# Kernel optimization log

Hardware: AMD Instinct MI355X
Metric: run time of the kernel (lower is better)

Reference implementation:

```python
import jax, jax.numpy as jnp
import numpy as np


def setup_inputs() -> dict:
    key = jax.random.key(0)
    ks = jax.random.split(key, 5)
    S, B, H, L = 512, 64, 1024, 2
    scale = 0.1
    return {
        "x": jax.random.normal(ks[0], (S, B, H), dtype=jnp.float32),
        "h0": jnp.zeros((L, B, H), dtype=jnp.float32),
        "c0": jnp.zeros((L, B, H), dtype=jnp.float32),
        "Wx": jax.random.uniform(ks[1], (L, 4 * H, H), minval=-scale, maxval=scale, dtype=jnp.float32),
        "Wh": jax.random.uniform(ks[2], (L, 4 * H, H), minval=-scale, maxval=scale, dtype=jnp.float32),
        "bx": jax.random.uniform(ks[3], (L, 4 * H), minval=-scale, maxval=scale, dtype=jnp.float32),
        "bh": jax.random.uniform(ks[4], (L, 4 * H), minval=-scale, maxval=scale, dtype=jnp.float32),
    }


def _cell(x_t, h_prev, c_prev, Wx_l, Wh_l, bx_l, bh_l, H):
    # gates: [B, 4H]; chunk order per source: f, i, o, c_ex
    gates = x_t @ Wx_l.T + bx_l + h_prev @ Wh_l.T + bh_l
    f, i, o, c_ex = jnp.split(gates, 4, axis=1)
    f = jax.nn.sigmoid(f)
    i = jax.nn.sigmoid(i)
    o = jax.nn.sigmoid(o)
    c_ex = jnp.tanh(c_ex)
    c = f * c_prev + i * c_ex
    h = o * jnp.tanh(c)
    return h, c


def reference(x, h0, c0, Wx, Wh, bx, bh):
    # x: [S, B, H]; h0/c0: [L, B, H]; Wx/Wh: [L, 4H, H]; bx/bh: [L, 4H]
    L = h0.shape[0]
    H = h0.shape[-1]

    def step(carry, x_t):
        h_all, c_all = carry  # each [L, B, H]
        out = x_t
        hs, cs = [], []
        for l in range(L):  # small fixed layer count
            h, c = _cell(out, h_all[l], c_all[l], Wx[l], Wh[l], bx[l], bh[l], H)
            out = h  # dropout is identity in eval mode
            hs.append(h)
            cs.append(c)
        return (jnp.stack(hs, 0), jnp.stack(cs, 0)), out

    (h_fin, c_fin), ys = jax.lax.scan(step, (h0, c0), x)
    return ys, (h_fin, c_fin)
```

## Files before the change

kernel.cpp:

```cpp
#include <hip/hip_runtime.h>

typedef __bf16 bf16_t;
typedef __bf16 bf16x8 __attribute__((ext_vector_type(8)));
typedef __bf16 bf16x4 __attribute__((ext_vector_type(4)));
typedef float  f32x4  __attribute__((ext_vector_type(4)));
typedef unsigned long long u64;

#define S_LEN 512
#define BATCH 64
#define HID 1024
#define BH (BATCH*HID)
#define G4 (4*HID)
#define NBLK 256
#define LBLK 128
#define NTHR 512
#define CSTRIDE 16

__device__ __forceinline__ float sigmoid_f(float x) { return 1.f / (1.f + __expf(-x)); }
__device__ __forceinline__ float tanh_f(float x) {
    float e = __expf(-2.f * fabsf(x));
    float t = (1.f - e) / (1.f + e);
    return x >= 0.f ? t : -t;
}

__device__ __forceinline__ bf16x8 cvt8(const float* p) {
    float4 a = *reinterpret_cast<const float4*>(p);
    float4 b = *reinterpret_cast<const float4*>(p + 4);
    bf16x8 r;
    r[0] = (bf16_t)a.x; r[1] = (bf16_t)a.y; r[2] = (bf16_t)a.z; r[3] = (bf16_t)a.w;
    r[4] = (bf16_t)b.x; r[5] = (bf16_t)b.y; r[6] = (bf16_t)b.z; r[7] = (bf16_t)b.w;
    return r;
}

__device__ __forceinline__ void wait_layer(const unsigned* w, unsigned thr, int lane) {
    const unsigned* p0 = w + (size_t)lane * CSTRIDE;
    const unsigned* p1 = w + (size_t)(64 + lane) * CSTRIDE;
    for (;;) {
        unsigned a = __hip_atomic_load(p0, __ATOMIC_RELAXED, __HIP_MEMORY_SCOPE_AGENT);
        unsigned b = __hip_atomic_load(p1, __ATOMIC_RELAXED, __HIP_MEMORY_SCOPE_AGENT);
        if (__all((int)(a >= thr && b >= thr))) break;
        __builtin_amdgcn_s_sleep(1);
    }
    asm volatile("" ::: "memory");
}

__device__ __forceinline__ void wait_dual(const unsigned* w0, unsigned thr0,
                                          const unsigned* w1, unsigned thr1, int lane) {
    const unsigned* p00 = w0 + (size_t)lane * CSTRIDE;
    const unsigned* p01 = w0 + (size_t)(64 + lane) * CSTRIDE;
    const unsigned* p10 = w1 + (size_t)lane * CSTRIDE;
    const unsigned* p11 = w1 + (size_t)(64 + lane) * CSTRIDE;
    for (;;) {
        unsigned a = __hip_atomic_load(p00, __ATOMIC_RELAXED, __HIP_MEMORY_SCOPE_AGENT);
        unsigned b = __hip_atomic_load(p01, __ATOMIC_RELAXED, __HIP_MEMORY_SCOPE_AGENT);
        unsigned c = __hip_atomic_load(p10, __ATOMIC_RELAXED, __HIP_MEMORY_SCOPE_AGENT);
        unsigned d = __hip_atomic_load(p11, __ATOMIC_RELAXED, __HIP_MEMORY_SCOPE_AGENT);
        if (__all((int)(a >= thr0 && b >= thr0 && c >= thr1 && d >= thr1))) break;
        __builtin_amdgcn_s_sleep(1);
    }
    asm volatile("" ::: "memory");
}

__global__ void prep_kernel(const float* __restrict__ h0,
                            bf16_t* __restrict__ h0buf, bf16_t* __restrict__ h1buf,
                            unsigned* __restrict__ dw, int mask0, int mask1) {
    int gtid = blockIdx.x * blockDim.x + threadIdx.x;
    int gsz  = gridDim.x * blockDim.x;
    if (gtid < 2 * LBLK) dw[gtid * CSTRIDE] = 0u;
    for (int i = gtid; i < BH; i += gsz) {
        h0buf[(size_t)mask0 * BH + i] = (bf16_t)h0[i];
        h1buf[(size_t)mask1 * BH + i] = (bf16_t)h0[BH + i];
    }
}

__global__ __launch_bounds__(NTHR, 2) void lstm_persistent(
    const float* __restrict__ x,
    const float* __restrict__ c0,
    const float* __restrict__ Wx,
    const float* __restrict__ Wh,
    const float* __restrict__ bx,
    const float* __restrict__ bh,
    float* __restrict__ out,
    bf16_t* __restrict__ h0buf,
    bf16_t* __restrict__ h1buf,
    unsigned* __restrict__ dw,
    int ff, int mask0, int mask1)
{
    __shared__ __attribute__((aligned(16))) unsigned char lds_w[256 * 512];
    __shared__ __attribute__((aligned(16))) float lds_red[8 * 256];
    __shared__ __attribute__((aligned(16))) float lds_hf[BATCH * 8];

    const int tid  = threadIdx.x;
    const int bid  = blockIdx.x;
    const int l    = bid >> 7;
    const int ug8  = bid & 127;
    const int lane = tid & 63;
    const int wv   = tid >> 6;
    const int mt   = wv >> 1;
    const int kh   = wv & 1;
    const int quad = lane >> 4;
    const int r16  = lane & 15;

    float* ys   = out;
    float* hfin = out + (size_t)S_LEN * BH;
    float* cfin = hfin + 2 * BH;

    {
        const float* WxL = Wx + (size_t)l * G4 * HID;
        const float* WhL = Wh + (size_t)l * G4 * HID;
        for (int ch = tid; ch < 32 * 256; ch += NTHR) {
            int row = ch & 31;
            int gr  = ch >> 5;
            int ul = row >> 2, g = row & 3;
            size_t R = (size_t)g * HID + 8 * ug8 + ul;
            const float* src = (gr < 128) ? (WxL + R * HID + (size_t)gr * 8)
                                          : (WhL + R * HID + (size_t)(gr - 128) * 8);
            *reinterpret_cast<bf16x8*>(&lds_w[gr * 512 + row * 16]) = cvt8(src);
        }
    }

    const int b_loc  = lane >> 2;
    const int uu     = lane & 3;
    const int b_glob = 16 * mt + b_loc;
    const int u_loc  = 4 * kh + uu;
    const int u_glob = 8 * ug8 + u_loc;

    float bias_r[4];
    #pragma unroll
    for (int gi = 0; gi < 4; ++gi) {
        int R = gi * HID + u_glob;
        bias_r[gi] = bx[l * G4 + R] + bh[l * G4 + R];
    }
    float c_reg = c0[(size_t)l * BH + (size_t)b_glob * HID + u_glob];

    bf16_t* pubbuf = (l == 0) ? h0buf : h1buf;
    const int pubmask = (l == 0) ? mask0 : mask1;
    const unsigned* dw0 = dw;
    const unsigned* dw1 = dw + LBLK * CSTRIDE;
    unsigned* myword = &dw[(l * LBLK + ug8) * CSTRIDE];
    __syncthreads();

    const int arow_off = (16 * mt + r16) * HID + kh * 512 + quad * 8;

    bf16x8 axp[16];
    if (l == 0) {
        const float* arow = x + arow_off;
        #pragma unroll
        for (int ks = 0; ks < 16; ++ks) axp[ks] = cvt8(arow + ks * 32);
    }

    for (int t = 0; t < S_LEN; ++t) {
        f32x4 acc0 = {0.f, 0.f, 0.f, 0.f};
        f32x4 acc1 = {0.f, 0.f, 0.f, 0.f};

        if (l == 0) {
            #pragma unroll
            for (int ks = 0; ks < 16; ++ks) {
                int gr = kh * 64 + ks * 4 + quad;
                bf16x8 b0 = *reinterpret_cast<const bf16x8*>(&lds_w[gr * 512 + r16 * 16]);
                bf16x8 b1 = *reinterpret_cast<const bf16x8*>(&lds_w[gr * 512 + (16 + r16) * 16]);
                acc0 = __builtin_amdgcn_mfma_f32_16x16x32_bf16(axp[ks], b0, acc0, 0, 0, 0);
                acc1 = __builtin_amdgcn_mfma_f32_16x16x32_bf16(axp[ks], b1, acc1, 0, 0, 0);
            }
            if (t + 1 < S_LEN) {
                const float* arow = x + (size_t)(t + 1) * BH + arow_off;
                #pragma unroll
                for (int ks = 0; ks < 16; ++ks) axp[ks] = cvt8(arow + ks * 32);
            }
            wait_layer(dw0, (unsigned)t, lane);
            if (!ff) __builtin_amdgcn_fence(__ATOMIC_ACQUIRE, "agent");
            const bf16_t* ah = h0buf + (size_t)((t - 1) & mask0) * BH + arow_off;
            bf16x8 af[16];
            #pragma unroll
            for (int ks = 0; ks < 16; ++ks)
                af[ks] = *reinterpret_cast<const bf16x8*>(ah + ks * 32);
            #pragma unroll
            for (int ks = 0; ks < 16; ++ks) {
                int gr = 128 + kh * 64 + ks * 4 + quad;
                bf16x8 b0 = *reinterpret_cast<const bf16x8*>(&lds_w[gr * 512 + r16 * 16]);
                bf16x8 b1 = *reinterpret_cast<const bf16x8*>(&lds_w[gr * 512 + (16 + r16) * 16]);
                acc0 = __builtin_amdgcn_mfma_f32_16x16x32_bf16(af[ks], b0, acc0, 0, 0, 0);
                acc1 = __builtin_amdgcn_mfma_f32_16x16x32_bf16(af[ks], b1, acc1, 0, 0, 0);
            }
        } else {
            wait_dual(dw0, (unsigned)(t + 1), dw1, (unsigned)t, lane);
            if (!ff) __builtin_amdgcn_fence(__ATOMIC_ACQUIRE, "agent");
            const bf16_t* ah = h1buf + (size_t)((t - 1) & mask1) * BH + arow_off;
            const bf16_t* ax = h0buf + (size_t)(t & mask0) * BH + arow_off;
            bf16x8 ahf[16], axf[16];
            #pragma unroll
            for (int ks = 0; ks < 16; ++ks)
                ahf[ks] = *reinterpret_cast<const bf16x8*>(ah + ks * 32);
            #pragma unroll
            for (int ks = 0; ks < 16; ++ks)
                axf[ks] = *reinterpret_cast<const bf16x8*>(ax + ks * 32);
            #pragma unroll
            for (int ks = 0; ks < 16; ++ks) {
                int gr = 128 + kh * 64 + ks * 4 + quad;
                bf16x8 b0 = *reinterpret_cast<const bf16x8*>(&lds_w[gr * 512 + r16 * 16]);
                bf16x8 b1 = *reinterpret_cast<const bf16x8*>(&lds_w[gr * 512 + (16 + r16) * 16]);
                acc0 = __builtin_amdgcn_mfma_f32_16x16x32_bf16(ahf[ks], b0, acc0, 0, 0, 0);
                acc1 = __builtin_amdgcn_mfma_f32_16x16x32_bf16(ahf[ks], b1, acc1, 0, 0, 0);
            }
            #pragma unroll
            for (int ks = 0; ks < 16; ++ks) {
                int gr = kh * 64 + ks * 4 + quad;
                bf16x8 b0 = *reinterpret_cast<const bf16x8*>(&lds_w[gr * 512 + r16 * 16]);
                bf16x8 b1 = *reinterpret_cast<const bf16x8*>(&lds_w[gr * 512 + (16 + r16) * 16]);
                acc0 = __builtin_amdgcn_mfma_f32_16x16x32_bf16(axf[ks], b0, acc0, 0, 0, 0);
                acc1 = __builtin_amdgcn_mfma_f32_16x16x32_bf16(axf[ks], b1, acc1, 0, 0, 0);
            }
        }

        {
            f32x4 ship = kh ? acc0 : acc1;
            *reinterpret_cast<f32x4*>(&lds_red[wv * 256 + lane * 4]) = ship;
            __syncthreads();
            f32x4 part = *reinterpret_cast<const f32x4*>(&lds_red[(wv ^ 1) * 256 + lane * 4]);
            f32x4 keep = kh ? acc1 : acc0;
            acc0 = keep + part;
        }

        {
            const int quad_s = b_loc >> 2;
            const int reg_s  = b_loc & 3;
            float gsum[4];
            #pragma unroll
            for (int gi = 0; gi < 4; ++gi) {
                int lane_s = (quad_s << 4) | (4 * uu + gi);
                float v0 = __shfl(acc0[0], lane_s, 64);
                float v1 = __shfl(acc0[1], lane_s, 64);
                float v2 = __shfl(acc0[2], lane_s, 64);
                float v3 = __shfl(acc0[3], lane_s, 64);
                float v  = (reg_s == 0) ? v0 : (reg_s == 1) ? v1 : (reg_s == 2) ? v2 : v3;
                gsum[gi] = v + bias_r[gi];
            }
            float fg = sigmoid_f(gsum[0]);
            float ig = sigmoid_f(gsum[1]);
            float og = sigmoid_f(gsum[2]);
            float cx = tanh_f(gsum[3]);
            float cN = fg * c_reg + ig * cx;
            float h  = og * tanh_f(cN);
            c_reg = cN;
            lds_hf[b_glob * 8 + u_loc] = h;
            if (t == S_LEN - 1) {
                hfin[(size_t)l * BH + (size_t)b_glob * HID + u_glob] = h;
                cfin[(size_t)l * BH + (size_t)b_glob * HID + u_glob] = cN;
            }
        }
        __syncthreads();

        if (tid < 64) {
            if (!ff && l == 0 && t >= 8) {
                const unsigned thr = (unsigned)(t - 6);
                for (;;) {
                    unsigned v0 = __hip_atomic_load(&dw1[lane * CSTRIDE],
                                                    __ATOMIC_RELAXED, __HIP_MEMORY_SCOPE_AGENT);
                    unsigned v1 = __hip_atomic_load(&dw1[(64 + lane) * CSTRIDE],
                                                    __ATOMIC_RELAXED, __HIP_MEMORY_SCOPE_AGENT);
                    if (__all((int)(v0 >= thr && v1 >= thr))) break;
                    __builtin_amdgcn_s_sleep(1);
                }
            }
            const float* hp = &lds_hf[lane * 8];
            union { bf16x4 v; u64 q; } p0, p1;
            #pragma unroll
            for (int j = 0; j < 4; ++j) {
                p0.v[j] = (bf16_t)hp[j];
                p1.v[j] = (bf16_t)hp[4 + j];
            }
            bf16_t* dst = pubbuf + (size_t)(t & pubmask) * BH + (size_t)lane * HID + 8 * ug8;
            __hip_atomic_store((u64*)(void*)dst,       p0.q, __ATOMIC_RELAXED, __HIP_MEMORY_SCOPE_AGENT);
            __hip_atomic_store((u64*)(void*)(dst + 4), p1.q, __ATOMIC_RELAXED, __HIP_MEMORY_SCOPE_AGENT);
            asm volatile("s_waitcnt vmcnt(0)" ::: "memory");
            if (lane == 0)
                __hip_atomic_store(myword, (unsigned)(t + 1),
                                   __ATOMIC_RELAXED, __HIP_MEMORY_SCOPE_AGENT);
            if (l == 1) {
                float* yd = ys + (size_t)t * BH + (size_t)lane * HID + 8 * ug8;
                __builtin_nontemporal_store(*reinterpret_cast<const f32x4*>(hp),     reinterpret_cast<f32x4*>(yd));
                __builtin_nontemporal_store(*reinterpret_cast<const f32x4*>(hp + 4), reinterpret_cast<f32x4*>(yd + 4));
            }
        }
    }
}

extern "C" void kernel_launch(void* const* d_in, const int* in_sizes, int n_in,
                              void* d_out, int out_size, void* d_ws, size_t ws_size,
                              hipStream_t stream) {
    (void)in_sizes; (void)n_in; (void)out_size;
    const float* x  = (const float*)d_in[0];
    const float* h0 = (const float*)d_in[1];
    const float* c0 = (const float*)d_in[2];
    const float* Wx = (const float*)d_in[3];
    const float* Wh = (const float*)d_in[4];
    const float* bx = (const float*)d_in[5];
    const float* bh = (const float*)d_in[6];

    unsigned char* ws = (unsigned char*)d_ws;
    unsigned* dw = (unsigned*)ws;
    size_t off = 32768;
    size_t need_ff = off + (size_t)2 * S_LEN * BH * 2;
    int ff, mask0, mask1;
    bf16_t *h0buf, *h1buf;
    if (ws_size >= need_ff) {
        ff = 1; mask0 = S_LEN - 1; mask1 = S_LEN - 1;
        h0buf = (bf16_t*)(ws + off); off += (size_t)S_LEN * BH * 2;
        h1buf = (bf16_t*)(ws + off);
    } else {
        ff = 0; mask0 = 7; mask1 = 1;
        h0buf = (bf16_t*)(ws + off); off += (size_t)8 * BH * 2;
        h1buf = (bf16_t*)(ws + off);
    }

    prep_kernel<<<2048, 256, 0, stream>>>(h0, h0buf, h1buf, dw, mask0, mask1);
    lstm_persistent<<<NBLK, NTHR, 0, stream>>>(x, c0, Wx, Wh, bx, bh, (float*)d_out,
                                               h0buf, h1buf, dw, ff, mask0, mask1);
}
```

Measured before the change: 6.746 ms.

## Centralize inter-block flag polling in one wave and pack flags densely

Counter flags are packed contiguously instead of padded to 64-byte strides, so a poll touches fewer cache lines. A single wave now polls all global readiness flags and releases the rest of the block through an LDS generation word, where before every wave polled global memory. The layer-0 backpressure wait on layer 1 moves from the publish phase into this same pre-step poll. This cuts global atomic polling traffic, but the other waves now spin on LDS and rely on LDS ordering, and writers of neighbouring flags now share cache lines.

```diff
diff --git a/kernel.cpp b/kernel.cpp
--- a/kernel.cpp
+++ b/kernel.cpp
@@ -14,7 +14,6 @@
 #define NBLK 256
 #define LBLK 128
 #define NTHR 512
-#define CSTRIDE 16
 
 __device__ __forceinline__ float sigmoid_f(float x) { return 1.f / (1.f + __expf(-x)); }
 __device__ __forceinline__ float tanh_f(float x) {
@@ -32,41 +31,12 @@
     return r;
 }
 
-__device__ __forceinline__ void wait_layer(const unsigned* w, unsigned thr, int lane) {
-    const unsigned* p0 = w + (size_t)lane * CSTRIDE;
-    const unsigned* p1 = w + (size_t)(64 + lane) * CSTRIDE;
-    for (;;) {
-        unsigned a = __hip_atomic_load(p0, __ATOMIC_RELAXED, __HIP_MEMORY_SCOPE_AGENT);
-        unsigned b = __hip_atomic_load(p1, __ATOMIC_RELAXED, __HIP_MEMORY_SCOPE_AGENT);
-        if (__all((int)(a >= thr && b >= thr))) break;
-        __builtin_amdgcn_s_sleep(1);
-    }
-    asm volatile("" ::: "memory");
-}
-
-__device__ __forceinline__ void wait_dual(const unsigned* w0, unsigned thr0,
-                                          const unsigned* w1, unsigned thr1, int lane) {
-    const unsigned* p00 = w0 + (size_t)lane * CSTRIDE;
-    const unsigned* p01 = w0 + (size_t)(64 + lane) * CSTRIDE;
-    const unsigned* p10 = w1 + (size_t)lane * CSTRIDE;
-    const unsigned* p11 = w1 + (size_t)(64 + lane) * CSTRIDE;
-    for (;;) {
-        unsigned a = __hip_atomic_load(p00, __ATOMIC_RELAXED, __HIP_MEMORY_SCOPE_AGENT);
-        unsigned b = __hip_atomic_load(p01, __ATOMIC_RELAXED, __HIP_MEMORY_SCOPE_AGENT);
-        unsigned c = __hip_atomic_load(p10, __ATOMIC_RELAXED, __HIP_MEMORY_SCOPE_AGENT);
-        unsigned d = __hip_atomic_load(p11, __ATOMIC_RELAXED, __HIP_MEMORY_SCOPE_AGENT);
-        if (__all((int)(a >= thr0 && b >= thr0 && c >= thr1 && d >= thr1))) break;
-        __builtin_amdgcn_s_sleep(1);
-    }
-    asm volatile("" ::: "memory");
-}
-
 __global__ void prep_kernel(const float* __restrict__ h0,
                             bf16_t* __restrict__ h0buf, bf16_t* __restrict__ h1buf,
                             unsigned* __restrict__ dw, int mask0, int mask1) {
     int gtid = blockIdx.x * blockDim.x + threadIdx.x;
     int gsz  = gridDim.x * blockDim.x;
-    if (gtid < 2 * LBLK) dw[gtid * CSTRIDE] = 0u;
+    if (gtid < 2 * LBLK) dw[gtid] = 0u;
     for (int i = gtid; i < BH; i += gsz) {
         h0buf[(size_t)mask0 * BH + i] = (bf16_t)h0[i];
         h1buf[(size_t)mask1 * BH + i] = (bf16_t)h0[BH + i];
@@ -89,6 +59,7 @@
     __shared__ __attribute__((aligned(16))) unsigned char lds_w[256 * 512];
     __shared__ __attribute__((aligned(16))) float lds_red[8 * 256];
     __shared__ __attribute__((aligned(16))) float lds_hf[BATCH * 8];
+    __shared__ unsigned lds_go;
 
     const int tid  = threadIdx.x;
     const int bid  = blockIdx.x;
@@ -104,6 +75,8 @@
     float* ys   = out;
     float* hfin = out + (size_t)S_LEN * BH;
     float* cfin = hfin + 2 * BH;
+
+    if (tid == 0) lds_go = 0u;
 
     {
         const float* WxL = Wx + (size_t)l * G4 * HID;
@@ -136,8 +109,8 @@
     bf16_t* pubbuf = (l == 0) ? h0buf : h1buf;
     const int pubmask = (l == 0) ? mask0 : mask1;
     const unsigned* dw0 = dw;
-    const unsigned* dw1 = dw + LBLK * CSTRIDE;
-    unsigned* myword = &dw[(l * LBLK + ug8) * CSTRIDE];
+    const unsigned* dw1 = dw + LBLK;
+    unsigned* myword = &dw[l * LBLK + ug8];
     __syncthreads();
 
     const int arow_off = (16 * mt + r16) * HID + kh * 512 + quad * 8;
@@ -152,6 +125,7 @@
     for (int t = 0; t < S_LEN; ++t) {
         f32x4 acc0 = {0.f, 0.f, 0.f, 0.f};
         f32x4 acc1 = {0.f, 0.f, 0.f, 0.f};
+        const unsigned gen = (unsigned)t + 1u;
 
         if (l == 0) {
             #pragma unroll
@@ -167,8 +141,39 @@
                 #pragma unroll
                 for (int ks = 0; ks < 16; ++ks) axp[ks] = cvt8(arow + ks * 32);
             }
-            wait_layer(dw0, (unsigned)t, lane);
-            if (!ff) __builtin_amdgcn_fence(__ATOMIC_ACQUIRE, "agent");
+        }
+
+        if (wv == 7) {
+            unsigned thr0, thr1;
+            if (l == 0) {
+                thr0 = (unsigned)t;
+                thr1 = (!ff && t >= 8) ? (unsigned)(t - 6) : 0u;
+            } else {
+                thr0 = (unsigned)(t + 1);
+                thr1 = (unsigned)t;
+            }
+            const unsigned* q0 = dw0 + lane;
+            const unsigned* q1 = dw0 + 64 + lane;
+            const unsigned* q2 = dw1 + lane;
+            const unsigned* q3 = dw1 + 64 + lane;
+            for (;;) {
+                unsigned a = __hip_atomic_load(q0, __ATOMIC_RELAXED, __HIP_MEMORY_SCOPE_AGENT);
+                unsigned b = __hip_atomic_load(q1, __ATOMIC_RELAXED, __HIP_MEMORY_SCOPE_AGENT);
+                unsigned c = __hip_atomic_load(q2, __ATOMIC_RELAXED, __HIP_MEMORY_SCOPE_AGENT);
+                unsigned d = __hip_atomic_load(q3, __ATOMIC_RELAXED, __HIP_MEMORY_SCOPE_AGENT);
+                if (__all((int)(a >= thr0 && b >= thr0 && c >= thr1 && d >= thr1))) break;
+                __builtin_amdgcn_s_sleep(1);
+            }
+            __hip_atomic_store(&lds_go, gen, __ATOMIC_RELAXED, __HIP_MEMORY_SCOPE_WORKGROUP);
+        } else {
+            while (__hip_atomic_load(&lds_go, __ATOMIC_RELAXED,
+                                     __HIP_MEMORY_SCOPE_WORKGROUP) < gen)
+                __builtin_amdgcn_s_sleep(1);
+        }
+        asm volatile("" ::: "memory");
+        if (!ff) __builtin_amdgcn_fence(__ATOMIC_ACQUIRE, "agent");
+
+        if (l == 0) {
             const bf16_t* ah = h0buf + (size_t)((t - 1) & mask0) * BH + arow_off;
             bf16x8 af[16];
             #pragma unroll
@@ -183,8 +188,6 @@
                 acc1 = __builtin_amdgcn_mfma_f32_16x16x32_bf16(af[ks], b1, acc1, 0, 0, 0);
             }
         } else {
-            wait_dual(dw0, (unsigned)(t + 1), dw1, (unsigned)t, lane);
-            if (!ff) __builtin_amdgcn_fence(__ATOMIC_ACQUIRE, "agent");
             const bf16_t* ah = h1buf + (size_t)((t - 1) & mask1) * BH + arow_off;
             const bf16_t* ax = h0buf + (size_t)(t & mask0) * BH + arow_off;
             bf16x8 ahf[16], axf[16];
@@ -251,17 +254,6 @@
         __syncthreads();
 
         if (tid < 64) {
-            if (!ff && l == 0 && t >= 8) {
-                const unsigned thr = (unsigned)(t - 6);
-                for (;;) {
-                    unsigned v0 = __hip_atomic_load(&dw1[lane * CSTRIDE],
-                                                    __ATOMIC_RELAXED, __HIP_MEMORY_SCOPE_AGENT);
-                    unsigned v1 = __hip_atomic_load(&dw1[(64 + lane) * CSTRIDE],
-                                                    __ATOMIC_RELAXED, __HIP_MEMORY_SCOPE_AGENT);
-                    if (__all((int)(v0 >= thr && v1 >= thr))) break;
-                    __builtin_amdgcn_s_sleep(1);
-                }
-            }
             const float* hp = &lds_hf[lane * 8];
             union { bf16x4 v; u64 q; } p0, p1;
             #pragma unroll
@@ -274,8 +266,7 @@
             __hip_atomic_store((u64*)(void*)(dst + 4), p1.q, __ATOMIC_RELAXED, __HIP_MEMORY_SCOPE_AGENT);
             asm volatile("s_waitcnt vmcnt(0)" ::: "memory");
             if (lane == 0)
-                __hip_atomic_store(myword, (unsigned)(t + 1),
-                                   __ATOMIC_RELAXED, __HIP_MEMORY_SCOPE_AGENT);
+                __hip_atomic_store(myword, gen, __ATOMIC_RELAXED, __HIP_MEMORY_SCOPE_AGENT);
             if (l == 1) {
                 float* yd = ys + (size_t)t * BH + (size_t)lane * HID + 8 * ug8;
                 __builtin_nontemporal_store(*reinterpret_cast<const f32x4*>(hp),     reinterpret_cast<f32x4*>(yd));
```

Result: slower. 7.551 ms (+11.9%).

## Move layer-1 back-pressure wait and ys stores off the publish critical path

Applied to the files above, without the earlier changes.

Folds layer 0's ring-buffer back-pressure wait on layer 1 into the existing pre-GEMM dual wait, so the single publishing wave no longer spins after the barrier. Each layer-1 thread keeps its h value and writes ys for the previous step after the loads of the next step are issued, so the output stores overlap with the next step's MFMA work instead of delaying the publish path. It also shrinks the flag stride and reorders the x prefetch after the h loads, with sched barriers to pin the order. Risks include extra shuffles, flags sharing cache lines now that the stride is smaller, and ordering subtleties in the added wait.

```diff
diff --git a/kernel.cpp b/kernel.cpp
--- a/kernel.cpp
+++ b/kernel.cpp
@@ -14,7 +14,7 @@
 #define NBLK 256
 #define LBLK 128
 #define NTHR 512
-#define CSTRIDE 16
+#define CSTRIDE 4
 
 __device__ __forceinline__ float sigmoid_f(float x) { return 1.f / (1.f + __expf(-x)); }
 __device__ __forceinline__ float tanh_f(float x) {
@@ -148,10 +148,12 @@
         #pragma unroll
         for (int ks = 0; ks < 16; ++ks) axp[ks] = cvt8(arow + ks * 32);
     }
+    float h_prev = 0.f;
 
     for (int t = 0; t < S_LEN; ++t) {
         f32x4 acc0 = {0.f, 0.f, 0.f, 0.f};
         f32x4 acc1 = {0.f, 0.f, 0.f, 0.f};
+        const unsigned gen = (unsigned)t + 1u;
 
         if (l == 0) {
             #pragma unroll
@@ -162,18 +164,21 @@
                 acc0 = __builtin_amdgcn_mfma_f32_16x16x32_bf16(axp[ks], b0, acc0, 0, 0, 0);
                 acc1 = __builtin_amdgcn_mfma_f32_16x16x32_bf16(axp[ks], b1, acc1, 0, 0, 0);
             }
+            unsigned thrg = (!ff && t >= 8) ? (unsigned)(t - 6) : 0u;
+            if (thrg) wait_dual(dw0, (unsigned)t, dw1, thrg, lane);
+            else      wait_layer(dw0, (unsigned)t, lane);
+            if (!ff) __builtin_amdgcn_fence(__ATOMIC_ACQUIRE, "agent");
+            const bf16_t* ah = h0buf + (size_t)((t - 1) & mask0) * BH + arow_off;
+            bf16x8 af[16];
+            #pragma unroll
+            for (int ks = 0; ks < 16; ++ks)
+                af[ks] = *reinterpret_cast<const bf16x8*>(ah + ks * 32);
             if (t + 1 < S_LEN) {
                 const float* arow = x + (size_t)(t + 1) * BH + arow_off;
                 #pragma unroll
                 for (int ks = 0; ks < 16; ++ks) axp[ks] = cvt8(arow + ks * 32);
             }
-            wait_layer(dw0, (unsigned)t, lane);
-            if (!ff) __builtin_amdgcn_fence(__ATOMIC_ACQUIRE, "agent");
-            const bf16_t* ah = h0buf + (size_t)((t - 1) & mask0) * BH + arow_off;
-            bf16x8 af[16];
-            #pragma unroll
-            for (int ks = 0; ks < 16; ++ks)
-                af[ks] = *reinterpret_cast<const bf16x8*>(ah + ks * 32);
+            __builtin_amdgcn_sched_barrier(0);
             #pragma unroll
             for (int ks = 0; ks < 16; ++ks) {
                 int gr = 128 + kh * 64 + ks * 4 + quad;
@@ -194,6 +199,19 @@
             #pragma unroll
             for (int ks = 0; ks < 16; ++ks)
                 axf[ks] = *reinterpret_cast<const bf16x8*>(ax + ks * 32);
+            if (t > 0) {
+                f32x4 yv;
+                yv[0] = h_prev;
+                yv[1] = __shfl_xor(h_prev, 1, 64);
+                yv[2] = __shfl_xor(h_prev, 2, 64);
+                yv[3] = __shfl_xor(h_prev, 3, 64);
+                if (uu == 0) {
+                    float* yd = ys + (size_t)(t - 1) * BH + (size_t)b_glob * HID
+                              + 8 * ug8 + 4 * kh;
+                    __builtin_nontemporal_store(yv, reinterpret_cast<f32x4*>(yd));
+                }
+            }
+            __builtin_amdgcn_sched_barrier(0);
             #pragma unroll
             for (int ks = 0; ks < 16; ++ks) {
                 int gr = 128 + kh * 64 + ks * 4 + quad;
@@ -242,6 +260,7 @@
             float cN = fg * c_reg + ig * cx;
             float h  = og * tanh_f(cN);
             c_reg = cN;
+            h_prev = h;
             lds_hf[b_glob * 8 + u_loc] = h;
             if (t == S_LEN - 1) {
                 hfin[(size_t)l * BH + (size_t)b_glob * HID + u_glob] = h;
@@ -251,17 +270,6 @@
         __syncthreads();
 
         if (tid < 64) {
-            if (!ff && l == 0 && t >= 8) {
-                const unsigned thr = (unsigned)(t - 6);
-                for (;;) {
-                    unsigned v0 = __hip_atomic_load(&dw1[lane * CSTRIDE],
-                                                    __ATOMIC_RELAXED, __HIP_MEMORY_SCOPE_AGENT);
-                    unsigned v1 = __hip_atomic_load(&dw1[(64 + lane) * CSTRIDE],
-                                                    __ATOMIC_RELAXED, __HIP_MEMORY_SCOPE_AGENT);
-                    if (__all((int)(v0 >= thr && v1 >= thr))) break;
-                    __builtin_amdgcn_s_sleep(1);
-                }
-            }
             const float* hp = &lds_hf[lane * 8];
             union { bf16x4 v; u64 q; } p0, p1;
             #pragma unroll
@@ -274,13 +282,20 @@
             __hip_atomic_store((u64*)(void*)(dst + 4), p1.q, __ATOMIC_RELAXED, __HIP_MEMORY_SCOPE_AGENT);
             asm volatile("s_waitcnt vmcnt(0)" ::: "memory");
             if (lane == 0)
-                __hip_atomic_store(myword, (unsigned)(t + 1),
-                                   __ATOMIC_RELAXED, __HIP_MEMORY_SCOPE_AGENT);
-            if (l == 1) {
-                float* yd = ys + (size_t)t * BH + (size_t)lane * HID + 8 * ug8;
-                __builtin_nontemporal_store(*reinterpret_cast<const f32x4*>(hp),     reinterpret_cast<f32x4*>(yd));
-                __builtin_nontemporal_store(*reinterpret_cast<const f32x4*>(hp + 4), reinterpret_cast<f32x4*>(yd + 4));
-            }
+                __hip_atomic_store(myword, gen, __ATOMIC_RELAXED, __HIP_MEMORY_SCOPE_AGENT);
+        }
+    }
+
+    if (l == 1) {
+        f32x4 yv;
+        yv[0] = h_prev;
+        yv[1] = __shfl_xor(h_prev, 1, 64);
+        yv[2] = __shfl_xor(h_prev, 2, 64);
+        yv[3] = __shfl_xor(h_prev, 3, 64);
+        if (uu == 0) {
+            float* yd = ys + (size_t)(S_LEN - 1) * BH + (size_t)b_glob * HID
+                      + 8 * ug8 + 4 * kh;
+            __builtin_nontemporal_store(yv, reinterpret_cast<f32x4*>(yd));
         }
     }
 }
```

Result: slower. 9.483 ms (+40.6%).
